# Optimization experiments

Measured on AMD Instinct MI355X. Metric: run time of the kernel, lower is better.

Reference implementation:

```python
import jax, jax.numpy as jnp
import numpy as np
import math

N_HEADS = 16
EPS = 1e-6


def rmsnorm(x, w):
    xf = x.astype(jnp.float32)
    n = xf * jax.lax.rsqrt(jnp.mean(xf * xf, axis=-1, keepdims=True) + EPS)
    return n.astype(x.dtype) * w


def setup_inputs() -> dict:
    key = jax.random.key(0)
    ks = jax.random.split(key, 8)
    B, T, C, Hf = 1, 4096, 1024, 4096
    s = lambda fan_in: 1.0 / math.sqrt(fan_in)
    return {
        "x": jax.random.normal(ks[0], (B, T, C), jnp.float32),
        "attn_norm_w": jnp.ones((C,), jnp.float32),
        "ffn_norm_w": jnp.ones((C,), jnp.float32),
        "c_attn_w": jax.random.normal(ks[1], (3 * C, C), jnp.float32) * s(C),
        "c_proj_w": jax.random.normal(ks[2], (C, C), jnp.float32) * s(C),
        "w1": jax.random.normal(ks[3], (Hf, C), jnp.float32) * s(C),
        "w2": jax.random.normal(ks[4], (C, Hf), jnp.float32) * s(Hf),
        "w3": jax.random.normal(ks[5], (Hf, C), jnp.float32) * s(C),
    }


def attention(x, c_attn_w, c_proj_w):
    B, T, C = x.shape
    hd = C // N_HEADS
    qkv = x @ c_attn_w.T  # [B,T,3C]
    q, k, v = jnp.split(qkv, 3, axis=-1)
    q = q.reshape(B, T, N_HEADS, hd).transpose(0, 2, 1, 3)  # [B,H,T,hd]
    k = k.reshape(B, T, N_HEADS, hd).transpose(0, 2, 1, 3)
    v = v.reshape(B, T, N_HEADS, hd).transpose(0, 2, 1, 3)
    att = jnp.einsum('bhqd,bhkd->bhqk', q, k) * (1.0 / math.sqrt(hd))
    mask = jnp.tril(jnp.ones((T, T), bool))  # causal
    att = jnp.where(mask, att, -jnp.inf)
    att = jax.nn.softmax(att, axis=-1)
    y = jnp.einsum('bhqk,bhkd->bhqd', att, v)
    y = y.transpose(0, 2, 1, 3).reshape(B, T, C)
    return y @ c_proj_w.T


def ffn(x, w1, w2, w3):
    return (jax.nn.silu(x @ w1.T) * (x @ w3.T)) @ w2.T


def reference(x, attn_norm_w, ffn_norm_w, c_attn_w, c_proj_w, w1, w2, w3):
    x = x + attention(rmsnorm(x, attn_norm_w), c_attn_w, c_proj_w)
    x = x + ffn(rmsnorm(x, ffn_norm_w), w1, w2, w3)
    return x
```

## Files before the change

### kernel.cpp

```cpp
#include <hip/hip_runtime.h>
#include <hip/hip_bf16.h>

typedef __hip_bfloat16 bf16;
typedef __bf16 bf16r;
typedef bf16r bf16x8 __attribute__((ext_vector_type(8)));
typedef bf16r bf16x4 __attribute__((ext_vector_type(4)));
typedef float f32x4 __attribute__((ext_vector_type(4)));

#define T_SEQ 4096
#define C_DIM 1024
#define LD_QKV 3072
#define MB(x) ((size_t)(x) << 20)
#define SCL 0.18033688011112042f

static __device__ __forceinline__ unsigned short f2bf(float f) {
    bf16 h = (bf16)f;
    return *reinterpret_cast<unsigned short*>(&h);
}

__global__ __launch_bounds__(256) void cvt_w(const float* __restrict__ src, size_t eoff,
                                             ushort4* __restrict__ dst, int n4,
                                             int n4scl, float scl) {
    int i = blockIdx.x * 256 + threadIdx.x;
    const int stride = gridDim.x * 256;
    const float4* s = (const float4*)(src + eoff);
    for (; i < n4; i += stride) {
        float4 v = s[i];
        const float m = (i < n4scl) ? scl : 1.0f;
        ushort4 o;
        o.x = f2bf(v.x * m); o.y = f2bf(v.y * m); o.z = f2bf(v.z * m); o.w = f2bf(v.w * m);
        dst[i] = o;
    }
}

__global__ __launch_bounds__(256) void cvt_w2h(const float* __restrict__ src, int coff,
                                               ushort4* __restrict__ dst) {
    const int i = blockIdx.x * 256 + threadIdx.x;
    const int row = i >> 9;
    const int c4 = i & 511;
    float4 v = *(const float4*)(src + (size_t)row * 4096 + coff + c4 * 4);
    ushort4 o;
    o.x = f2bf(v.x); o.y = f2bf(v.y); o.z = f2bf(v.z); o.w = f2bf(v.w);
    dst[i] = o;
}

__global__ __launch_bounds__(256) void copy_f32(const float4* __restrict__ src,
                                                float4* __restrict__ dst, int n4) {
    int i = blockIdx.x * 256 + threadIdx.x;
    const int stride = gridDim.x * 256;
    for (; i < n4; i += stride) dst[i] = src[i];
}

__global__ __launch_bounds__(256) void rmsnorm_k(const float* __restrict__ x,
                                                 const float* __restrict__ w,
                                                 bf16* __restrict__ out) {
    const int row = blockIdx.x;
    const int tid = threadIdx.x;
    const float* xr = x + (size_t)row * C_DIM;
    float v[4];
    float ss = 0.f;
#pragma unroll
    for (int i = 0; i < 4; i++) { v[i] = xr[tid * 4 + i]; ss += v[i] * v[i]; }
#pragma unroll
    for (int off = 32; off; off >>= 1) ss += __shfl_xor(ss, off);
    __shared__ float red[4];
    if ((tid & 63) == 0) red[tid >> 6] = ss;
    __syncthreads();
    const float tot = red[0] + red[1] + red[2] + red[3];
    const float scale = rsqrtf(tot * (1.0f / C_DIM) + 1e-6f);
#pragma unroll
    for (int i = 0; i < 4; i++) {
        const int c = tid * 4 + i;
        out[(size_t)row * C_DIM + c] = (bf16)(v[i] * scale * w[c]);
    }
}

template <int RESID, int OUTF32>
__global__ __launch_bounds__(256) void gemm128(const bf16* __restrict__ A, int lda,
                                               const bf16* __restrict__ B, int ldb,
                                               const void* __restrict__ resid,
                                               void* __restrict__ out,
                                               int N, int K) {
    __shared__ __align__(16) bf16r As[128 * 32];
    __shared__ __align__(16) bf16r Bs[128 * 32];
    const int tid = threadIdx.x;
    const int w = tid >> 6, lane = tid & 63;
    const int c = lane & 15, qd = lane >> 4;
    const int wm = w >> 1, wn = w & 1;
    const int mbase = blockIdx.y * 128;
    const int nbase = blockIdx.x * 128;
    const size_t koff = (size_t)blockIdx.z * K;

    const int srow = lane >> 2, schk = lane & 3;
    const bf16* gA = A + (size_t)(mbase + w * 32 + srow) * lda + schk * 8 + koff;
    const bf16* gB = B + (size_t)(nbase + w * 32 + srow) * ldb + schk * 8 + koff;

    f32x4 acc[4][4] = {};

    for (int k0 = 0; k0 < K; k0 += 32) {
        __syncthreads();
#pragma unroll
        for (int s = 0; s < 2; s++) {
            __builtin_amdgcn_global_load_lds(
                (const __attribute__((address_space(1))) void*)(gA + (size_t)(s * 16) * lda + k0),
                (__attribute__((address_space(3))) void*)&As[(w * 32 + s * 16) * 32], 16, 0, 0);
            __builtin_amdgcn_global_load_lds(
                (const __attribute__((address_space(1))) void*)(gB + (size_t)(s * 16) * ldb + k0),
                (__attribute__((address_space(3))) void*)&Bs[(w * 32 + s * 16) * 32], 16, 0, 0);
        }
        __syncthreads();

        bf16x8 a[4], b[4];
#pragma unroll
        for (int i = 0; i < 4; i++)
            a[i] = *(const bf16x8*)&As[(wm * 64 + i * 16 + c) * 32 + qd * 8];
#pragma unroll
        for (int j = 0; j < 4; j++)
            b[j] = *(const bf16x8*)&Bs[(wn * 64 + j * 16 + c) * 32 + qd * 8];
#pragma unroll
        for (int i = 0; i < 4; i++)
#pragma unroll
            for (int j = 0; j < 4; j++)
                acc[i][j] = __builtin_amdgcn_mfma_f32_16x16x32_bf16(a[i], b[j], acc[i][j], 0, 0, 0);
    }

#pragma unroll
    for (int i = 0; i < 4; i++) {
#pragma unroll
        for (int j = 0; j < 4; j++) {
            const int col = nbase + wn * 64 + j * 16 + c;
#pragma unroll
            for (int reg = 0; reg < 4; reg++) {
                const int row = mbase + wm * 64 + i * 16 + qd * 4 + reg;
                const size_t idx = (size_t)row * N + col;
                float v = acc[i][j][reg];
                if (RESID == 2) v += ((const float*)resid)[idx];
                if (RESID == 3) {
                    const float a1 = (float)((const bf16*)resid)[idx];
                    v = (a1 / (1.0f + __expf(-a1))) * v;
                }
                if (RESID == 4) {
                    atomicAdd(&((float*)out)[idx], v);
                } else if (OUTF32) {
                    ((float*)out)[idx] = v;
                } else {
                    ((bf16*)out)[idx] = (bf16)v;
                }
            }
        }
    }
}

__global__ __launch_bounds__(256, 2) void gemm_w13(const bf16* __restrict__ A,
                                                   const bf16* __restrict__ B1,
                                                   const bf16* __restrict__ B3,
                                                   bf16* __restrict__ out,
                                                   int N, int K) {
    __shared__ __align__(16) bf16r As[128 * 32];
    __shared__ __align__(16) bf16r B1s[128 * 32];
    __shared__ __align__(16) bf16r B3s[128 * 32];
    const int tid = threadIdx.x;
    const int w = tid >> 6, lane = tid & 63;
    const int c = lane & 15, qd = lane >> 4;
    const int wm = w >> 1, wn = w & 1;
    const int mbase = blockIdx.y * 128;
    const int nbase = blockIdx.x * 128;

    const int srow = lane >> 2, schk = lane & 3;
    const bf16* gA = A + (size_t)(mbase + w * 32 + srow) * K + schk * 8;
    const bf16* gB1 = B1 + (size_t)(nbase + w * 32 + srow) * K + schk * 8;
    const bf16* gB3 = B3 + (size_t)(nbase + w * 32 + srow) * K + schk * 8;

    f32x4 acc1[4][4] = {};
    f32x4 acc3[4][4] = {};

    for (int k0 = 0; k0 < K; k0 += 32) {
        __syncthreads();
#pragma unroll
        for (int s = 0; s < 2; s++) {
            __builtin_amdgcn_global_load_lds(
                (const __attribute__((address_space(1))) void*)(gA + (size_t)(s * 16) * K + k0),
                (__attribute__((address_space(3))) void*)&As[(w * 32 + s * 16) * 32], 16, 0, 0);
            __builtin_amdgcn_global_load_lds(
                (const __attribute__((address_space(1))) void*)(gB1 + (size_t)(s * 16) * K + k0),
                (__attribute__((address_space(3))) void*)&B1s[(w * 32 + s * 16) * 32], 16, 0, 0);
            __builtin_amdgcn_global_load_lds(
                (const __attribute__((address_space(1))) void*)(gB3 + (size_t)(s * 16) * K + k0),
                (__attribute__((address_space(3))) void*)&B3s[(w * 32 + s * 16) * 32], 16, 0, 0);
        }
        __syncthreads();

        bf16x8 a[4], b1[4], b3[4];
#pragma unroll
        for (int i = 0; i < 4; i++)
            a[i] = *(const bf16x8*)&As[(wm * 64 + i * 16 + c) * 32 + qd * 8];
#pragma unroll
        for (int j = 0; j < 4; j++) {
            b1[j] = *(const bf16x8*)&B1s[(wn * 64 + j * 16 + c) * 32 + qd * 8];
            b3[j] = *(const bf16x8*)&B3s[(wn * 64 + j * 16 + c) * 32 + qd * 8];
        }
#pragma unroll
        for (int i = 0; i < 4; i++)
#pragma unroll
            for (int j = 0; j < 4; j++) {
                acc1[i][j] = __builtin_amdgcn_mfma_f32_16x16x32_bf16(a[i], b1[j], acc1[i][j], 0, 0, 0);
                acc3[i][j] = __builtin_amdgcn_mfma_f32_16x16x32_bf16(a[i], b3[j], acc3[i][j], 0, 0, 0);
            }
    }

#pragma unroll
    for (int i = 0; i < 4; i++) {
#pragma unroll
        for (int j = 0; j < 4; j++) {
            const int col = nbase + wn * 64 + j * 16 + c;
#pragma unroll
            for (int reg = 0; reg < 4; reg++) {
                const int row = mbase + wm * 64 + i * 16 + qd * 4 + reg;
                const float a1 = acc1[i][j][reg];
                const float h = (a1 / (1.0f + __expf(-a1))) * acc3[i][j][reg];
                out[(size_t)row * N + col] = (bf16)h;
            }
        }
    }
}

__global__ __launch_bounds__(256) void build_tr(const bf16* __restrict__ qkv,
                                                bf16* __restrict__ dst, int soff) {
    const int h = blockIdx.y;
    const int tb = blockIdx.x;
    __shared__ bf16 tile[64][65];
    const int tx = threadIdx.x & 63;
    const int ty = threadIdx.x >> 6;
    for (int rr = ty; rr < 64; rr += 4)
        tile[rr][tx] = qkv[(size_t)(tb * 64 + rr) * LD_QKV + soff + h * 64 + tx];
    __syncthreads();
    for (int rr = ty; rr < 64; rr += 4)
        dst[((size_t)h * 64 + rr) * T_SEQ + tb * 64 + tx] = tile[tx][rr];
}

#define CTR_STRIDE 16
__global__ void zero_ctr(int* p) { if (threadIdx.x < 8 * CTR_STRIDE) p[threadIdx.x] = 0; }

__global__ __launch_bounds__(256) void attn_mfma(const bf16* __restrict__ qkv,
                                                 const bf16* __restrict__ VT,
                                                 bf16* __restrict__ y,
                                                 int* __restrict__ ctrs) {
    __shared__ __align__(16) bf16r Ks[128][64];
    __shared__ __align__(16) bf16r VTs[64][128];
    __shared__ __align__(16) bf16r Ps[4][16][128];
    __shared__ int s_wi;

    const int tid  = threadIdx.x;
    const int w    = tid >> 6;
    const int lane = tid & 63;
    const int c    = lane & 15;
    const int qd   = lane >> 4;
    const int sw   = c & 7;
    const int qi   = blockIdx.x & 7;
    int* ctr = ctrs + qi * CTR_STRIDE;

    while (true) {
        __syncthreads();
        if (tid == 0) s_wi = atomicAdd(ctr, 1);
        __syncthreads();
        const int j = s_wi;
        if (j >= 128) break;

        const int h    = qi + 8 * (j & 1);
        const int qb   = 63 - (j >> 1);
        const int qrow = qb * 64 + w * 16 + c;

        bf16x8 qf[2];
        {
            const bf16* qp = qkv + (size_t)qrow * LD_QKV + h * 64;
            qf[0] = *(const bf16x8*)(qp + qd * 8);
            qf[1] = *(const bf16x8*)(qp + 32 + qd * 8);
        }

        f32x4 O[4] = {};
        float m_i = -1e30f, l_i = 0.f;
        const int nkb = (qb >> 1) + 1;

        for (int kb = 0; kb < nkb; kb++) {
            __syncthreads();
#pragma unroll
            for (int ii = 0; ii < 4; ii++) {
                const int i = ii * 256 + tid;
                const int kr = i >> 3, ch = i & 7;
                *(bf16x8*)&Ks[kr][(ch ^ (kr & 7)) * 8] =
                    *(const bf16x8*)(qkv + (size_t)(kb * 128 + kr) * LD_QKV + C_DIM + h * 64 + ch * 8);
                const int vr = i >> 4, vch = i & 15;
                *(bf16x8*)&VTs[vr][(vch ^ (vr & 7)) * 8] =
                    *(const bf16x8*)(VT + ((size_t)h * 64 + vr) * T_SEQ + kb * 128 + vch * 8);
            }
            __syncthreads();

            f32x4 ST[8];
#pragma unroll
            for (int kt = 0; kt < 8; kt++) {
                f32x4 z = {};
#pragma unroll
                for (int ks = 0; ks < 2; ks++) {
                    bf16x8 kf = *(const bf16x8*)&Ks[kt * 16 + c][((ks * 4 + qd) ^ sw) * 8];
                    z = __builtin_amdgcn_mfma_f32_16x16x32_bf16(kf, qf[ks], z, 0, 0, 0);
                }
                ST[kt] = z;
            }

            if (kb == nkb - 1) {
#pragma unroll
                for (int kt = 0; kt < 8; kt++)
#pragma unroll
                    for (int r = 0; r < 4; r++)
                        if (kb * 128 + kt * 16 + qd * 4 + r > qrow) ST[kt][r] = -1e30f;
            }

            float mb = -1e30f;
#pragma unroll
            for (int kt = 0; kt < 8; kt++)
#pragma unroll
                for (int r = 0; r < 4; r++) mb = fmaxf(mb, ST[kt][r]);
            mb = fmaxf(mb, __shfl_xor(mb, 16));
            mb = fmaxf(mb, __shfl_xor(mb, 32));

            bf16x4 pv[8];
            float rs = 0.f;
            if (__all(mb - m_i <= 8.0f)) {
#pragma unroll
                for (int kt = 0; kt < 8; kt++)
#pragma unroll
                    for (int r = 0; r < 4; r++) {
                        const float p = exp2f(ST[kt][r] - m_i);
                        pv[kt][r] = (bf16r)p;
                        rs += p;
                    }
                rs += __shfl_xor(rs, 16);
                rs += __shfl_xor(rs, 32);
                l_i += rs;
            } else {
                const float mnew = fmaxf(m_i, mb);
                const float alpha = exp2f(m_i - mnew);
#pragma unroll
                for (int kt = 0; kt < 8; kt++)
#pragma unroll
                    for (int r = 0; r < 4; r++) {
                        const float p = exp2f(ST[kt][r] - mnew);
                        pv[kt][r] = (bf16r)p;
                        rs += p;
                    }
                rs += __shfl_xor(rs, 16);
                rs += __shfl_xor(rs, 32);
                l_i = l_i * alpha + rs;
                m_i = mnew;
#pragma unroll
                for (int dt = 0; dt < 4; dt++)
#pragma unroll
                    for (int r = 0; r < 4; r++) O[dt][r] *= alpha;
            }

#pragma unroll
            for (int kt = 0; kt < 8; kt++) {
                const int phys = (kt * 2 + (qd >> 1)) ^ sw;
                *(bf16x4*)&Ps[w][c][phys * 8 + (qd & 1) * 4] = pv[kt];
            }

#pragma unroll
            for (int ks = 0; ks < 4; ks++) {
                bf16x8 pf = *(const bf16x8*)&Ps[w][c][((ks * 4 + qd) ^ sw) * 8];
#pragma unroll
                for (int dt = 0; dt < 4; dt++) {
                    bf16x8 vf = *(const bf16x8*)&VTs[dt * 16 + c][((ks * 4 + qd) ^ sw) * 8];
                    O[dt] = __builtin_amdgcn_mfma_f32_16x16x32_bf16(vf, pf, O[dt], 0, 0, 0);
                }
            }
        }

        const float inv_l = 1.0f / l_i;
#pragma unroll
        for (int dt = 0; dt < 4; dt++) {
            bf16x4 ov;
#pragma unroll
            for (int r = 0; r < 4; r++) ov[r] = (bf16r)(O[dt][r] * inv_l);
            *(bf16x4*)(y + (size_t)qrow * C_DIM + h * 64 + dt * 16 + qd * 4) = ov;
        }
    }
}

extern "C" void kernel_launch(void* const* d_in, const int* in_sizes, int n_in,
                              void* d_out, int out_size, void* d_ws, size_t ws_size,
                              hipStream_t stream) {
    const float* x        = (const float*)d_in[0];
    const float* attn_w   = (const float*)d_in[1];
    const float* ffn_w    = (const float*)d_in[2];
    const float* c_attn_w = (const float*)d_in[3];
    const float* c_proj_w = (const float*)d_in[4];
    const float* w1       = (const float*)d_in[5];
    const float* w2       = (const float*)d_in[6];
    const float* w3       = (const float*)d_in[7];
    float* xmid = (float*)d_out;

    char* ws = (char*)d_ws;
    bf16* cwA = (bf16*)(ws);
    bf16* cwP = (bf16*)(ws + MB(6));
    bf16* rms = (bf16*)(ws + MB(8));
    bf16* qkv = (bf16*)(ws + MB(16));
    bf16* VT  = (bf16*)(ws + MB(40));
    bf16* y   = (bf16*)(ws + MB(48));
    bf16* w1h = (bf16*)(ws + MB(16));
    bf16* w3h = (bf16*)(ws + MB(20));
    bf16* w2h = (bf16*)(ws + MB(24));
    bf16* h1h = (bf16*)(ws + MB(28));
    int* ctrs = (int*)(ws + MB(8));

    cvt_w<<<512, 256, 0, stream>>>(c_attn_w, 0, (ushort4*)cwA, 3072 * 1024 / 4,
                                   1024 * 1024 / 4, SCL);
    cvt_w<<<512, 256, 0, stream>>>(c_proj_w, 0, (ushort4*)cwP, 1024 * 1024 / 4, 0, 1.0f);
    rmsnorm_k<<<T_SEQ, 256, 0, stream>>>(x, attn_w, rms);
    gemm128<0, 0><<<dim3(24, 32), 256, 0, stream>>>(rms, C_DIM, cwA, C_DIM, nullptr, qkv, 3072, 1024);
    build_tr<<<dim3(64, 16), 256, 0, stream>>>(qkv, VT, 2 * C_DIM);
    zero_ctr<<<1, 128, 0, stream>>>(ctrs);
    attn_mfma<<<768, 256, 0, stream>>>(qkv, VT, y, ctrs);
    copy_f32<<<2048, 256, 0, stream>>>((const float4*)x, (float4*)xmid, T_SEQ * C_DIM / 4);
    gemm128<4, 1><<<dim3(8, 32, 2), 256, 0, stream>>>(y, C_DIM, cwP, C_DIM, nullptr, xmid, 1024, 512);
    rmsnorm_k<<<T_SEQ, 256, 0, stream>>>(xmid, ffn_w, rms);
    for (int hh = 0; hh < 2; hh++) {
        cvt_w<<<512, 256, 0, stream>>>(w1, (size_t)hh * 2048 * 1024, (ushort4*)w1h,
                                       2048 * 1024 / 4, 0, 1.0f);
        cvt_w<<<512, 256, 0, stream>>>(w3, (size_t)hh * 2048 * 1024, (ushort4*)w3h,
                                       2048 * 1024 / 4, 0, 1.0f);
        gemm_w13<<<dim3(16, 32), 256, 0, stream>>>(rms, w1h, w3h, h1h, 2048, 1024);
        cvt_w2h<<<2048, 256, 0, stream>>>(w2, hh * 2048, (ushort4*)w2h);
        gemm128<4, 1><<<dim3(8, 32, 2), 256, 0, stream>>>(h1h, 2048, w2h, 2048, nullptr, xmid, 1024, 1024);
    }
}
```

Measured before the change: 508.7 us.

## Use direct global-to-LDS loads in attention and unsplit the FFN into single GEMMs

Attention K/V tile staging now uses global_load_lds so data goes straight into shared memory instead of through registers. The swizzle moves onto the global address side, and an explicit vmcnt wait is added. The FFN no longer processes the hidden dimension in two halves. It converts w1/w3/w2 in full, runs one w1/w3 GEMM over all 4096 hidden units and one down-projection with split-K of 4, and drops the per-half w2 column conversion kernel. The workspace is re-laid out so the larger buffers fit, reusing regions freed after attention; this risks aliasing errors if lifetimes overlap.

```diff
diff --git a/kernel.cpp b/kernel.cpp
--- a/kernel.cpp
+++ b/kernel.cpp
@@ -31,17 +31,6 @@
         o.x = f2bf(v.x * m); o.y = f2bf(v.y * m); o.z = f2bf(v.z * m); o.w = f2bf(v.w * m);
         dst[i] = o;
     }
-}
-
-__global__ __launch_bounds__(256) void cvt_w2h(const float* __restrict__ src, int coff,
-                                               ushort4* __restrict__ dst) {
-    const int i = blockIdx.x * 256 + threadIdx.x;
-    const int row = i >> 9;
-    const int c4 = i & 511;
-    float4 v = *(const float4*)(src + (size_t)row * 4096 + coff + c4 * 4);
-    ushort4 o;
-    o.x = f2bf(v.x); o.y = f2bf(v.y); o.z = f2bf(v.z); o.w = f2bf(v.w);
-    dst[i] = o;
 }
 
 __global__ __launch_bounds__(256) void copy_f32(const float4* __restrict__ src,
@@ -259,6 +248,9 @@
     const int qi   = blockIdx.x & 7;
     int* ctr = ctrs + qi * CTR_STRIDE;
 
+    const int k_ri = lane >> 3, k_pc = lane & 7;
+    const int v_ri = lane >> 4, v_pc = lane & 15;
+
     while (true) {
         __syncthreads();
         if (tid == 0) s_wi = atomicAdd(ctr, 1);
@@ -285,14 +277,21 @@
             __syncthreads();
 #pragma unroll
             for (int ii = 0; ii < 4; ii++) {
-                const int i = ii * 256 + tid;
-                const int kr = i >> 3, ch = i & 7;
-                *(bf16x8*)&Ks[kr][(ch ^ (kr & 7)) * 8] =
-                    *(const bf16x8*)(qkv + (size_t)(kb * 128 + kr) * LD_QKV + C_DIM + h * 64 + ch * 8);
-                const int vr = i >> 4, vch = i & 15;
-                *(bf16x8*)&VTs[vr][(vch ^ (vr & 7)) * 8] =
-                    *(const bf16x8*)(VT + ((size_t)h * 64 + vr) * T_SEQ + kb * 128 + vch * 8);
-            }
+                const int grp = w * 4 + ii;
+                const int kr = grp * 8 + k_ri;
+                const int kch = k_pc ^ (kr & 7);
+                __builtin_amdgcn_global_load_lds(
+                    (const __attribute__((address_space(1))) void*)
+                        (qkv + (size_t)(kb * 128 + kr) * LD_QKV + C_DIM + h * 64 + kch * 8),
+                    (__attribute__((address_space(3))) void*)&Ks[grp * 8][0], 16, 0, 0);
+                const int vr = grp * 4 + v_ri;
+                const int vch = v_pc ^ (vr & 7);
+                __builtin_amdgcn_global_load_lds(
+                    (const __attribute__((address_space(1))) void*)
+                        (VT + ((size_t)h * 64 + vr) * T_SEQ + kb * 128 + vch * 8),
+                    (__attribute__((address_space(3))) void*)&VTs[grp * 4][0], 16, 0, 0);
+            }
+            asm volatile("s_waitcnt vmcnt(0)" ::: "memory");
             __syncthreads();
 
             f32x4 ST[8];
@@ -400,36 +399,33 @@
     float* xmid = (float*)d_out;
 
     char* ws = (char*)d_ws;
-    bf16* cwA = (bf16*)(ws);
-    bf16* cwP = (bf16*)(ws + MB(6));
-    bf16* rms = (bf16*)(ws + MB(8));
-    bf16* qkv = (bf16*)(ws + MB(16));
-    bf16* VT  = (bf16*)(ws + MB(40));
-    bf16* y   = (bf16*)(ws + MB(48));
-    bf16* w1h = (bf16*)(ws + MB(16));
-    bf16* w3h = (bf16*)(ws + MB(20));
-    bf16* w2h = (bf16*)(ws + MB(24));
-    bf16* h1h = (bf16*)(ws + MB(28));
-    int* ctrs = (int*)(ws + MB(8));
+    bf16* cwA  = (bf16*)(ws);
+    bf16* cwP  = (bf16*)(ws + MB(6));
+    bf16* rms1 = (bf16*)(ws + MB(8));
+    bf16* qkv  = (bf16*)(ws + MB(16));
+    bf16* VT   = (bf16*)(ws + MB(40));
+    bf16* y    = (bf16*)(ws + MB(48));
+    int*  ctrs = (int*)(ws + MB(8));
+    bf16* rms2 = (bf16*)(ws);
+    bf16* w1h  = (bf16*)(ws + MB(8));
+    bf16* w3h  = (bf16*)(ws + MB(16));
+    bf16* w2h  = (bf16*)(ws + MB(8));
+    bf16* h1   = (bf16*)(ws + MB(24));
 
     cvt_w<<<512, 256, 0, stream>>>(c_attn_w, 0, (ushort4*)cwA, 3072 * 1024 / 4,
                                    1024 * 1024 / 4, SCL);
     cvt_w<<<512, 256, 0, stream>>>(c_proj_w, 0, (ushort4*)cwP, 1024 * 1024 / 4, 0, 1.0f);
-    rmsnorm_k<<<T_SEQ, 256, 0, stream>>>(x, attn_w, rms);
-    gemm128<0, 0><<<dim3(24, 32), 256, 0, stream>>>(rms, C_DIM, cwA, C_DIM, nullptr, qkv, 3072, 1024);
+    rmsnorm_k<<<T_SEQ, 256, 0, stream>>>(x, attn_w, rms1);
+    gemm128<0, 0><<<dim3(24, 32), 256, 0, stream>>>(rms1, C_DIM, cwA, C_DIM, nullptr, qkv, 3072, 1024);
     build_tr<<<dim3(64, 16), 256, 0, stream>>>(qkv, VT, 2 * C_DIM);
     zero_ctr<<<1, 128, 0, stream>>>(ctrs);
     attn_mfma<<<768, 256, 0, stream>>>(qkv, VT, y, ctrs);
+    cvt_w<<<512, 256, 0, stream>>>(w1, 0, (ushort4*)w1h, 4096 * 1024 / 4, 0, 1.0f);
+    cvt_w<<<512, 256, 0, stream>>>(w3, 0, (ushort4*)w3h, 4096 * 1024 / 4, 0, 1.0f);
     copy_f32<<<2048, 256, 0, stream>>>((const float4*)x, (float4*)xmid, T_SEQ * C_DIM / 4);
     gemm128<4, 1><<<dim3(8, 32, 2), 256, 0, stream>>>(y, C_DIM, cwP, C_DIM, nullptr, xmid, 1024, 512);
-    rmsnorm_k<<<T_SEQ, 256, 0, stream>>>(xmid, ffn_w, rms);
-    for (int hh = 0; hh < 2; hh++) {
-        cvt_w<<<512, 256, 0, stream>>>(w1, (size_t)hh * 2048 * 1024, (ushort4*)w1h,
-                                       2048 * 1024 / 4, 0, 1.0f);
-        cvt_w<<<512, 256, 0, stream>>>(w3, (size_t)hh * 2048 * 1024, (ushort4*)w3h,
-                                       2048 * 1024 / 4, 0, 1.0f);
-        gemm_w13<<<dim3(16, 32), 256, 0, stream>>>(rms, w1h, w3h, h1h, 2048, 1024);
-        cvt_w2h<<<2048, 256, 0, stream>>>(w2, hh * 2048, (ushort4*)w2h);
-        gemm128<4, 1><<<dim3(8, 32, 2), 256, 0, stream>>>(h1h, 2048, w2h, 2048, nullptr, xmid, 1024, 1024);
-    }
-}
+    rmsnorm_k<<<T_SEQ, 256, 0, stream>>>(xmid, ffn_w, rms2);
+    gemm_w13<<<dim3(32, 32), 256, 0, stream>>>(rms2, w1h, w3h, h1, 4096, 1024);
+    cvt_w<<<512, 256, 0, stream>>>(w2, 0, (ushort4*)w2h, 1024 * 4096 / 4, 0, 1.0f);
+    gemm128<4, 1><<<dim3(8, 32, 4), 256, 0, stream>>>(h1, 4096, w2h, 4096, nullptr, xmid, 1024, 1024);
+}
```

New measurement: 499.1 us. About the same (-1.9%).
